# Kernel tuning notes

Measured on AMD Instinct MI355X. Metric: run time of the kernel, lower is better.

## Reference

```python
import jax, jax.numpy as jnp
import numpy as np

RADIUS = 5   # window half-width -> 11x11 window
OX = 4       # spatial gaussian sigma
OI = 10      # intensity gaussian sigma


def _distance_weights(p, ox, radius):
    # squared spatial distance within the (2p+1)^2 window, masked at dsq <= radius
    d = jnp.arange(2 * p + 1) - p
    dsq = (d[None, :] ** 2 + d[:, None] ** 2).astype(jnp.float32)
    mask = (dsq <= radius).astype(jnp.float32)
    return (jnp.exp(-dsq / (ox ** 2)) * mask).reshape(-1)  # [P]


def _patches(x, p):
    # x: [B, C, H, W] -> [B, C*P, H, W] with zero padding, P = (2p+1)^2
    kh = 2 * p + 1
    return jax.lax.conv_general_dilated_patches(
        x, (kh, kh), (1, 1), ((p, p), (p, p)))


def setup_inputs() -> dict:
    key = jax.random.key(0)
    k1, k2 = jax.random.split(key)
    image = jax.random.uniform(k1, (4, 3, 256, 256), dtype=jnp.float32)
    enc = jax.random.uniform(k2, (4, 4, 256, 256), dtype=jnp.float32)
    return {"image": image, "enc": enc}


def reference(image, enc):
    p = RADIUS
    kh = 2 * p + 1
    P = kh * kh
    B, _, H, W = image.shape
    k = enc.shape[1]

    # bilateral affinity weights from grayscale image
    img = jnp.mean(image, axis=1, keepdims=True)          # [B,1,H,W]
    ipat = _patches(img, p)                               # [B,P,H,W]
    center = ipat[:, p * kh + p][:, None]                 # [B,1,H,W]
    dw = _distance_weights(p, OX, RADIUS)                 # [P]
    weights = jnp.exp(-(ipat - center) ** 2 / (OI ** 2)) * dw[None, :, None, None]  # [B,P,H,W]

    # segmentation patches for all k channels at once
    segp = _patches(enc, p).reshape(B, k, P, H, W)        # [B,k,P,H,W]

    nom = jnp.einsum('bphw,bkphw->bkhw', weights, segp)   # sum over window
    numerator = jnp.sum(enc * nom, axis=(2, 3))           # [B,k]
    wsum = jnp.sum(weights, axis=1)                       # [B,H,W]
    denominator = jnp.sum(enc * wsum[:, None], axis=(2, 3))  # [B,k]

    loss_k = numerator / (denominator + 1e-8)             # [B,k]
    return jnp.mean(k - jnp.sum(loss_k, axis=1))
```

## Files before the change

kernel.cpp:

```cpp
#include <hip/hip_runtime.h>


#define TILE   32
#define HALO   2
#define TW     (TILE + 2 * HALO)
#define TP     (TW + 1)

__device__ __constant__ float c_dw5[5][5] = {
    {0.0f,        0.73161563f, 0.77880078f, 0.73161563f, 0.0f       },
    {0.73161563f, 0.88249690f, 0.93941306f, 0.88249690f, 0.73161563f},
    {0.77880078f, 0.93941306f, 1.00000000f, 0.93941306f, 0.77880078f},
    {0.73161563f, 0.88249690f, 0.93941306f, 0.88249690f, 0.73161563f},
    {0.0f,        0.73161563f, 0.77880078f, 0.73161563f, 0.0f       }};


__global__ __launch_bounds__(256) void snc_main(const float* __restrict__ img,
                                                const float* __restrict__ enc,
                                                float* __restrict__ part) {
    __shared__ float  sGray[TW * TP];
    __shared__ float4 sEnc [TW * TP];
    __shared__ float  red[4][8];

    const int b    = blockIdx.x >> 6;
    const int tile = blockIdx.x & 63;
    const int ph   = (tile >> 3) << 5;
    const int pw   = (tile & 7) << 5;

    const float* __restrict__ imgb = img + b * 3 * 65536;
    const float* __restrict__ encb = enc + b * 4 * 65536;

    const int tid = threadIdx.x;

    for (int i = tid; i < TW * TW; i += 256) {
        const int gy = i / TW;
        const int gx = i - gy * TW;
        const int hh = ph + gy - HALO;
        const int ww = pw + gx - HALO;
        const bool inb = ((unsigned)hh < 256u) && ((unsigned)ww < 256u);
        float g = 0.0f;
        float4 e = make_float4(0.0f, 0.0f, 0.0f, 0.0f);
        if (inb) {
            const int o = (hh << 8) | ww;
            g = (imgb[o] + imgb[65536 + o] + imgb[131072 + o]) * (1.0f / 3.0f);
            e.x = encb[o];
            e.y = encb[65536 + o];
            e.z = encb[131072 + o];
            e.w = encb[196608 + o];
        }
        sGray[gy * TP + gx] = g;
        sEnc [gy * TP + gx] = e;
    }
    __syncthreads();

    const int ly = tid >> 3;
    const int x0 = (tid & 7) << 2;
    const int cbase = (ly + HALO) * TP + (x0 + HALO);

    float  cg[4];
    float4 ce[4];
#pragma unroll
    for (int p = 0; p < 4; ++p) {
        cg[p] = sGray[cbase + p];
        ce[p] = sEnc [cbase + p];
    }

    float wsum[4], n0[4], n1[4], n2[4], n3[4];
#pragma unroll
    for (int p = 0; p < 4; ++p) { wsum[p] = n0[p] = n1[p] = n2[p] = n3[p] = 0.0f; }

#pragma unroll
    for (int r = -2; r <= 2; ++r) {
        const int lo = (r == -2 || r == 2) ? -1 : -2;
        const int base = (ly + HALO + r) * TP + (x0 + HALO);
#pragma unroll
        for (int dx = lo; dx <= 3 - lo; ++dx) {
            const float  g = sGray[base + dx];
            const float4 e = sEnc [base + dx];
#pragma unroll
            for (int p = 0; p < 4; ++p) {
                const int dc = dx - p;
                if (dc < -2 || dc > 2) continue;
                if (r * r + dc * dc > 5) continue;
                const float d  = g - cg[p];
                const float wg = __expf(d * d * -0.01f) * c_dw5[r + 2][dc + 2];
                wsum[p] += wg;
                n0[p] += wg * e.x;
                n1[p] += wg * e.y;
                n2[p] += wg * e.z;
                n3[p] += wg * e.w;
            }
        }
    }

    float v[8];
#pragma unroll
    for (int j = 0; j < 8; ++j) v[j] = 0.0f;
#pragma unroll
    for (int p = 0; p < 4; ++p) {
        v[0] += ce[p].x * n0[p];
        v[1] += ce[p].y * n1[p];
        v[2] += ce[p].z * n2[p];
        v[3] += ce[p].w * n3[p];
        v[4] += ce[p].x * wsum[p];
        v[5] += ce[p].y * wsum[p];
        v[6] += ce[p].z * wsum[p];
        v[7] += ce[p].w * wsum[p];
    }

#pragma unroll
    for (int off = 32; off; off >>= 1) {
#pragma unroll
        for (int j = 0; j < 8; ++j) v[j] += __shfl_down(v[j], off);
    }

    const int wave = tid >> 6;
    const int lane = tid & 63;
    if (lane == 0) {
#pragma unroll
        for (int j = 0; j < 8; ++j) red[wave][j] = v[j];
    }
    __syncthreads();

    if (tid < 8) {
        part[blockIdx.x * 8 + tid] =
            red[0][tid] + red[1][tid] + red[2][tid] + red[3][tid];
    }
}

__global__ __launch_bounds__(256) void snc_final(const float* __restrict__ part,
                                                 float* __restrict__ out) {
    const int t    = threadIdx.x;
    const int b    = t >> 6;
    const int lane = t & 63;

    const float4* p4 = (const float4*)(part + (size_t)(b * 64 + lane) * 8);
    const float4 a0 = p4[0];
    const float4 a1 = p4[1];
    float v[8] = {a0.x, a0.y, a0.z, a0.w, a1.x, a1.y, a1.z, a1.w};

#pragma unroll
    for (int off = 32; off; off >>= 1) {
#pragma unroll
        for (int j = 0; j < 8; ++j) v[j] += __shfl_down(v[j], off);
    }

    __shared__ float res[4];
    if (lane == 0) {
        float s = 0.0f;
#pragma unroll
        for (int k = 0; k < 4; ++k) s += v[k] / (v[4 + k] + 1e-8f);
        res[b] = 4.0f - s;
    }
    __syncthreads();
    if (t == 0) out[0] = (res[0] + res[1] + res[2] + res[3]) * 0.25f;
}

extern "C" void kernel_launch(void* const* d_in, const int* in_sizes, int n_in,
                              void* d_out, int out_size, void* d_ws, size_t ws_size,
                              hipStream_t stream) {
    const float* img = (const float*)d_in[0];
    const float* enc = (const float*)d_in[1];
    float* out  = (float*)d_out;
    float* part = (float*)d_ws;

    snc_main<<<dim3(256), dim3(256), 0, stream>>>(img, enc, part);
    snc_final<<<dim3(1), dim3(256), 0, stream>>>(part, out);
}
```

Before: 64.78 us.

## Use 32x16 tiles with two vertical pixels per thread and 512 blocks

```diff
diff --git a/kernel.cpp b/kernel.cpp
--- a/kernel.cpp
+++ b/kernel.cpp
@@ -1,10 +1,10 @@
 #include <hip/hip_runtime.h>
 
 
-#define TILE   32
 #define HALO   2
-#define TW     (TILE + 2 * HALO)
-#define TP     (TW + 1)
+#define TW     36
+#define TH     20
+#define TP     37
 
 __device__ __constant__ float c_dw5[5][5] = {
     {0.0f,        0.73161563f, 0.77880078f, 0.73161563f, 0.0f       },
@@ -14,16 +14,16 @@
     {0.0f,        0.73161563f, 0.77880078f, 0.73161563f, 0.0f       }};
 
 
-__global__ __launch_bounds__(256) void snc_main(const float* __restrict__ img,
-                                                const float* __restrict__ enc,
-                                                float* __restrict__ part) {
-    __shared__ float  sGray[TW * TP];
-    __shared__ float4 sEnc [TW * TP];
+__global__ __launch_bounds__(256, 2) void snc_main(const float* __restrict__ img,
+                                                   const float* __restrict__ enc,
+                                                   float* __restrict__ part) {
+    __shared__ float  sGray[TH * TP];
+    __shared__ float4 sEnc [TH * TP];
     __shared__ float  red[4][8];
 
-    const int b    = blockIdx.x >> 6;
-    const int tile = blockIdx.x & 63;
-    const int ph   = (tile >> 3) << 5;
+    const int b    = blockIdx.x >> 7;
+    const int tile = blockIdx.x & 127;
+    const int ph   = (tile >> 3) << 4;
     const int pw   = (tile & 7) << 5;
 
     const float* __restrict__ imgb = img + b * 3 * 65536;
@@ -31,7 +31,7 @@
 
     const int tid = threadIdx.x;
 
-    for (int i = tid; i < TW * TW; i += 256) {
+    for (int i = tid; i < TW * TH; i += 256) {
         const int gy = i / TW;
         const int gx = i - gy * TW;
         const int hh = ph + gy - HALO;
@@ -52,60 +52,60 @@
     }
     __syncthreads();
 
-    const int ly = tid >> 3;
-    const int x0 = (tid & 7) << 2;
-    const int cbase = (ly + HALO) * TP + (x0 + HALO);
+    const int x  = tid & 31;
+    const int y0 = (tid >> 5) << 1;
+    const int cb = (y0 + HALO) * TP + (x + HALO);
 
-    float  cg[4];
-    float4 ce[4];
-#pragma unroll
-    for (int p = 0; p < 4; ++p) {
-        cg[p] = sGray[cbase + p];
-        ce[p] = sEnc [cbase + p];
-    }
+    const float  cgA = sGray[cb];
+    const float  cgB = sGray[cb + TP];
+    const float4 ceA = sEnc [cb];
+    const float4 ceB = sEnc [cb + TP];
 
-    float wsum[4], n0[4], n1[4], n2[4], n3[4];
-#pragma unroll
-    for (int p = 0; p < 4; ++p) { wsum[p] = n0[p] = n1[p] = n2[p] = n3[p] = 0.0f; }
+    float wsA = 0.0f, a0 = 0.0f, a1 = 0.0f, a2 = 0.0f, a3 = 0.0f;
+    float wsB = 0.0f, b0 = 0.0f, b1 = 0.0f, b2 = 0.0f, b3 = 0.0f;
 
 #pragma unroll
-    for (int r = -2; r <= 2; ++r) {
-        const int lo = (r == -2 || r == 2) ? -1 : -2;
-        const int base = (ly + HALO + r) * TP + (x0 + HALO);
+    for (int rr = -2; rr <= 3; ++rr) {
+        const int lo = (rr == -2 || rr == 3) ? -1 : -2;
+        const int base = cb + rr * TP;
 #pragma unroll
-        for (int dx = lo; dx <= 3 - lo; ++dx) {
-            const float  g = sGray[base + dx];
-            const float4 e = sEnc [base + dx];
-#pragma unroll
-            for (int p = 0; p < 4; ++p) {
-                const int dc = dx - p;
-                if (dc < -2 || dc > 2) continue;
-                if (r * r + dc * dc > 5) continue;
-                const float d  = g - cg[p];
-                const float wg = __expf(d * d * -0.01f) * c_dw5[r + 2][dc + 2];
-                wsum[p] += wg;
-                n0[p] += wg * e.x;
-                n1[p] += wg * e.y;
-                n2[p] += wg * e.z;
-                n3[p] += wg * e.w;
+        for (int dc = lo; dc <= -lo; ++dc) {
+            const float  g = sGray[base + dc];
+            const float4 e = sEnc [base + dc];
+            if (rr >= -2 && rr <= 2 && rr * rr + dc * dc <= 5) {
+                if (rr == 0 && dc == 0) {
+                    wsA += 1.0f;
+                    a0 += e.x; a1 += e.y; a2 += e.z; a3 += e.w;
+                } else {
+                    const float d  = g - cgA;
+                    const float wg = __expf(d * d * -0.01f) * c_dw5[rr + 2][dc + 2];
+                    wsA += wg;
+                    a0 += wg * e.x; a1 += wg * e.y; a2 += wg * e.z; a3 += wg * e.w;
+                }
+            }
+            if ((rr - 1) >= -2 && (rr - 1) <= 2 && (rr - 1) * (rr - 1) + dc * dc <= 5) {
+                if ((rr - 1) == 0 && dc == 0) {
+                    wsB += 1.0f;
+                    b0 += e.x; b1 += e.y; b2 += e.z; b3 += e.w;
+                } else {
+                    const float d  = g - cgB;
+                    const float wg = __expf(d * d * -0.01f) * c_dw5[rr + 1][dc + 2];
+                    wsB += wg;
+                    b0 += wg * e.x; b1 += wg * e.y; b2 += wg * e.z; b3 += wg * e.w;
+                }
             }
         }
     }
 
     float v[8];
-#pragma unroll
-    for (int j = 0; j < 8; ++j) v[j] = 0.0f;
-#pragma unroll
-    for (int p = 0; p < 4; ++p) {
-        v[0] += ce[p].x * n0[p];
-        v[1] += ce[p].y * n1[p];
-        v[2] += ce[p].z * n2[p];
-        v[3] += ce[p].w * n3[p];
-        v[4] += ce[p].x * wsum[p];
-        v[5] += ce[p].y * wsum[p];
-        v[6] += ce[p].z * wsum[p];
-        v[7] += ce[p].w * wsum[p];
-    }
+    v[0] = ceA.x * a0 + ceB.x * b0;
+    v[1] = ceA.y * a1 + ceB.y * b1;
+    v[2] = ceA.z * a2 + ceB.z * b2;
+    v[3] = ceA.w * a3 + ceB.w * b3;
+    v[4] = ceA.x * wsA + ceB.x * wsB;
+    v[5] = ceA.y * wsA + ceB.y * wsB;
+    v[6] = ceA.z * wsA + ceB.z * wsB;
+    v[7] = ceA.w * wsA + ceB.w * wsB;
 
 #pragma unroll
     for (int off = 32; off; off >>= 1) {
@@ -133,10 +133,14 @@
     const int b    = t >> 6;
     const int lane = t & 63;
 
-    const float4* p4 = (const float4*)(part + (size_t)(b * 64 + lane) * 8);
-    const float4 a0 = p4[0];
-    const float4 a1 = p4[1];
-    float v[8] = {a0.x, a0.y, a0.z, a0.w, a1.x, a1.y, a1.z, a1.w};
+    const float4* p0 = (const float4*)(part + (size_t)(b * 128 + lane) * 8);
+    const float4* p1 = (const float4*)(part + (size_t)(b * 128 + 64 + lane) * 8);
+    const float4 a0 = p0[0];
+    const float4 a1 = p0[1];
+    const float4 c0 = p1[0];
+    const float4 c1 = p1[1];
+    float v[8] = {a0.x + c0.x, a0.y + c0.y, a0.z + c0.z, a0.w + c0.w,
+                  a1.x + c1.x, a1.y + c1.y, a1.z + c1.z, a1.w + c1.w};
 
 #pragma unroll
     for (int off = 32; off; off >>= 1) {
@@ -163,6 +167,6 @@
     float* out  = (float*)d_out;
     float* part = (float*)d_ws;
 
-    snc_main<<<dim3(256), dim3(256), 0, stream>>>(img, enc, part);
+    snc_main<<<dim3(512), dim3(256), 0, stream>>>(img, enc, part);
     snc_final<<<dim3(1), dim3(256), 0, stream>>>(part, out);
 }
```

After: 65.80 us. Within noise of the previous version (+1.6%).
